# Kernel optimization log

Hardware: AMD Instinct MI355X
Metric: run time of the kernel (lower is better)

The kernel has to match this reference:

```python
import jax, jax.numpy as jnp
import numpy as np

N_NODES = 50000


def setup_inputs() -> dict:
    key = jax.random.key(0)
    ks = jax.random.split(key, 6)
    nfeat, nhid, hops, nedges = 256, 64, 4, 800000
    x = jax.random.normal(ks[0], (N_NODES, nfeat), dtype=jnp.float32)
    W = jax.random.normal(ks[1], (hops, nfeat, nhid), dtype=jnp.float32) / np.sqrt(nfeat)
    b = jax.random.normal(ks[2], (hops, nhid), dtype=jnp.float32) * 0.01
    adj_rows = jax.random.randint(ks[3], (hops, nedges), 0, N_NODES, dtype=jnp.int32)
    adj_cols = jax.random.randint(ks[4], (hops, nedges), 0, N_NODES, dtype=jnp.int32)
    # normalize-ish positive edge weights, as in a GCN-normalized adjacency
    adj_vals = jax.random.uniform(ks[5], (hops, nedges), dtype=jnp.float32) / 16.0
    return {"x": x, "W": W, "b": b, "adj_rows": adj_rows,
            "adj_cols": adj_cols, "adj_vals": adj_vals}


def reference(x, W, b, adj_rows, adj_cols, adj_vals):
    # SIGN forward (eval mode: dropout = identity).
    # For each hop i: h = x @ W[i] + b[i]; out_i = spmm(adj_i, h)
    # spmm in COO form: out[r] = sum_{e: rows[e]==r} vals[e] * h[cols[e]]
    n = x.shape[0]
    hops = W.shape[0]
    outs = []
    for i in range(hops):  # small fixed hop count (layers+1)
        h = x @ W[i] + b[i]                      # [N, nhid] dense GEMM
        msgs = adj_vals[i][:, None] * h[adj_cols[i]]  # [E, nhid] gather
        outs.append(jax.ops.segment_sum(msgs, adj_rows[i], num_segments=n))
    return jax.nn.elu(jnp.concatenate(outs, axis=1))  # [N, hops*nhid]
```

## Files before the change

kernel.cpp:

```cpp
#include <hip/hip_runtime.h>
#include <hip/hip_bf16.h>
#include <math.h>

#define N_NODES 50000
#define NFEAT 256
#define NHID 64
#define HOPS 4
#define NEDGES 800000
#define NBINS (HOPS * N_NODES)

#define BROWS 64
#define NBUCK 782
#define NBK_ALL (HOPS * NBUCK)
#define CHUNK 4096
#define NCHUNK ((NEDGES + CHUNK - 1) / CHUNK)
#define FS_CAP 2048
#define MCAP 512

#define GM 64
#define LDP 40
#define NGBLK ((N_NODES + GM - 1) / GM)

#define PREP_BHIST (NCHUNK * HOPS)
#define PREP_CASTW_END (PREP_BHIST + 256)
#define PREP_CASTX_BLKS ((N_NODES * NFEAT / 8) / 256)
#define PREP_TOTAL (PREP_CASTW_END + PREP_CASTX_BLKS)

typedef short bf16x8 __attribute__((ext_vector_type(8)));
typedef float f32x4 __attribute__((ext_vector_type(4)));

static __device__ __forceinline__ unsigned short f2bf(float f) {
    __hip_bfloat16 h = __float2bfloat16(f);
    return *reinterpret_cast<unsigned short*>(&h);
}

__global__ __launch_bounds__(256) void prep_kernel(const float* __restrict__ x,
                                                   unsigned short* __restrict__ Xbf,
                                                   const float* __restrict__ W,
                                                   unsigned short* __restrict__ Wt,
                                                   const int* __restrict__ rows,
                                                   int* __restrict__ bucket_cnt) {
    __shared__ int h[NBUCK];
    const int bid = blockIdx.x;
    const int t = threadIdx.x;

    if (bid < PREP_BHIST) {
        for (int i = t; i < NBUCK; i += 256) h[i] = 0;
        __syncthreads();
        const int hop = bid / NCHUNK;
        const int e0 = (bid % NCHUNK) * CHUNK;
        const int n = min(CHUNK, NEDGES - e0);
        const size_t base = (size_t)hop * NEDGES + e0;
        for (int i = t; i < n; i += 256) {
            atomicAdd(&h[rows[base + i] >> 6], 1);
        }
        __syncthreads();
        for (int i = t; i < NBUCK; i += 256) {
            if (h[i]) atomicAdd(&bucket_cnt[hop * NBUCK + i], h[i]);
        }
    } else if (bid < PREP_CASTW_END) {
        const int idx = (bid - PREP_BHIST) * 256 + t;
        const int hop = idx >> 14;
        const int k = (idx >> 6) & 255;
        const int c = idx & 63;
        Wt[(size_t)(k >> 5) * (256 * 32) + (hop * 64 + c) * 32 + (k & 31)] = f2bf(W[idx]);
    } else {
        const size_t base = ((size_t)(bid - PREP_CASTW_END) * 256 + t) * 8;
        const float4 a = *(const float4*)&x[base];
        const float4 c = *(const float4*)&x[base + 4];
        unsigned short o[8] = {f2bf(a.x), f2bf(a.y), f2bf(a.z), f2bf(a.w),
                               f2bf(c.x), f2bf(c.y), f2bf(c.z), f2bf(c.w)};
        *(bf16x8*)&Xbf[base] = *(const bf16x8*)o;
    }
}

#define SCAN_V ((NBK_ALL + 255) / 256)
__global__ __launch_bounds__(256) void gemm_scan_kernel(const unsigned short* __restrict__ Xbf,
                                                        const unsigned short* __restrict__ Wt,
                                                        const float* __restrict__ b,
                                                        __hip_bfloat16* __restrict__ H,
                                                        const int* __restrict__ cnt,
                                                        int* __restrict__ start,
                                                        int* __restrict__ cursor,
                                                        int* __restrict__ offsets) {
    __shared__ char smem[GM * LDP * 2 + 256 * LDP * 2];
    const int t = threadIdx.x;

    if (blockIdx.x == 0) {
        int* s = (int*)smem;
        int v[SCAN_V];
        int tsum = 0;
#pragma unroll
        for (int i = 0; i < SCAN_V; ++i) {
            const int idx = t * SCAN_V + i;
            v[i] = (idx < NBK_ALL) ? cnt[idx] : 0;
            tsum += v[i];
        }
        s[t] = tsum;
        __syncthreads();
        for (int off = 1; off < 256; off <<= 1) {
            const int a = (t >= off) ? s[t - off] : 0;
            __syncthreads();
            s[t] += a;
            __syncthreads();
        }
        int run = s[t] - tsum;
#pragma unroll
        for (int i = 0; i < SCAN_V; ++i) {
            const int idx = t * SCAN_V + i;
            if (idx < NBK_ALL) {
                start[idx] = run;
                cursor[idx] = run;
                run += v[i];
            }
        }
        if (t == 255) {
            start[NBK_ALL] = run;
            offsets[NBINS] = run;
        }
        return;
    }

    unsigned short* A_lds = (unsigned short*)smem;
    unsigned short* B_lds = (unsigned short*)(smem + GM * LDP * 2);

    const int lane = t & 63;
    const int w = t >> 6;
    const int quad = lane >> 4;
    const int m16 = lane & 15;
    const int row0 = (blockIdx.x - 1) * GM;

    f32x4 acc[4][4];
#pragma unroll
    for (int mt = 0; mt < 4; ++mt)
#pragma unroll
        for (int nt = 0; nt < 4; ++nt) acc[mt][nt] = (f32x4){0.f, 0.f, 0.f, 0.f};

    for (int ks = 0; ks < 8; ++ks) {
        const int k0 = ks * 32;
        {
            const int r = t >> 2;
            const int kq = (t & 3) * 8;
            bf16x8 v = {0, 0, 0, 0, 0, 0, 0, 0};
            if (row0 + r < N_NODES)
                v = *(const bf16x8*)&Xbf[(size_t)(row0 + r) * NFEAT + k0 + kq];
            *(bf16x8*)&A_lds[r * LDP + kq] = v;
        }
#pragma unroll
        for (int it = 0; it < 4; ++it) {
            const int i = t + it * 256;
            const bf16x8 v = *(const bf16x8*)&Wt[(size_t)ks * (256 * 32) + (size_t)i * 8];
            *(bf16x8*)&B_lds[(i >> 2) * LDP + (i & 3) * 8] = v;
        }
        __syncthreads();

        bf16x8 af[4], bf[4];
#pragma unroll
        for (int mt = 0; mt < 4; ++mt)
            af[mt] = *(const bf16x8*)&A_lds[(mt * 16 + m16) * LDP + quad * 8];
#pragma unroll
        for (int nt = 0; nt < 4; ++nt)
            bf[nt] = *(const bf16x8*)&B_lds[(w * 64 + nt * 16 + m16) * LDP + quad * 8];
#pragma unroll
        for (int mt = 0; mt < 4; ++mt)
#pragma unroll
            for (int nt = 0; nt < 4; ++nt)
                acc[mt][nt] = __builtin_amdgcn_mfma_f32_16x16x32_bf16(
                    af[mt], bf[nt], acc[mt][nt], 0, 0, 0);
        __syncthreads();
    }

#pragma unroll
    for (int nt = 0; nt < 4; ++nt) {
        const int col = w * 64 + nt * 16 + m16;
        const float bias = b[col];
#pragma unroll
        for (int mt = 0; mt < 4; ++mt) {
#pragma unroll
            for (int r = 0; r < 4; ++r) {
                const int row = row0 + mt * 16 + quad * 4 + r;
                if (row < N_NODES)
                    H[(size_t)row * 256 + col] = __float2bfloat16(acc[mt][nt][r] + bias);
            }
        }
    }
}

__global__ __launch_bounds__(256) void gemm_mfma_kernel(const float* __restrict__ x,
                                                        const float* __restrict__ W,
                                                        const float* __restrict__ b,
                                                        __hip_bfloat16* __restrict__ H) {
    __shared__ unsigned short A_lds[GM * LDP];
    __shared__ unsigned short B_lds[256 * LDP];

    const int t = threadIdx.x;
    const int lane = t & 63;
    const int w = t >> 6;
    const int quad = lane >> 4;
    const int m16 = lane & 15;
    const int row0 = blockIdx.x * GM;

    f32x4 acc[4][4];
#pragma unroll
    for (int mt = 0; mt < 4; ++mt)
#pragma unroll
        for (int nt = 0; nt < 4; ++nt) acc[mt][nt] = (f32x4){0.f, 0.f, 0.f, 0.f};

    for (int ks = 0; ks < 8; ++ks) {
        const int k0 = ks * 32;
#pragma unroll
        for (int it = 0; it < 2; ++it) {
            const int i = t + it * 256;
            const int r = i >> 3;
            const int kq = (i & 7) * 4;
            float4 v = make_float4(0.f, 0.f, 0.f, 0.f);
            if (row0 + r < N_NODES)
                v = *(const float4*)&x[(size_t)(row0 + r) * NFEAT + k0 + kq];
            unsigned short* d = &A_lds[r * LDP + kq];
            d[0] = f2bf(v.x); d[1] = f2bf(v.y); d[2] = f2bf(v.z); d[3] = f2bf(v.w);
        }
#pragma unroll
        for (int it = 0; it < 8; ++it) {
            const int i = t + it * 256;
            const int n4 = i & 63;
            const int kk = i >> 6;
            const int hop = n4 >> 4;
            const int j = (n4 & 15) * 4;
            const float4 v = *(const float4*)&W[(size_t)hop * (NFEAT * NHID)
                                                + (size_t)(k0 + kk) * NHID + j];
            B_lds[(n4 * 4 + 0) * LDP + kk] = f2bf(v.x);
            B_lds[(n4 * 4 + 1) * LDP + kk] = f2bf(v.y);
            B_lds[(n4 * 4 + 2) * LDP + kk] = f2bf(v.z);
            B_lds[(n4 * 4 + 3) * LDP + kk] = f2bf(v.w);
        }
        __syncthreads();

        bf16x8 af[4], bf[4];
#pragma unroll
        for (int mt = 0; mt < 4; ++mt)
            af[mt] = *(const bf16x8*)&A_lds[(mt * 16 + m16) * LDP + quad * 8];
#pragma unroll
        for (int nt = 0; nt < 4; ++nt)
            bf[nt] = *(const bf16x8*)&B_lds[(w * 64 + nt * 16 + m16) * LDP + quad * 8];
#pragma unroll
        for (int mt = 0; mt < 4; ++mt)
#pragma unroll
            for (int nt = 0; nt < 4; ++nt)
                acc[mt][nt] = __builtin_amdgcn_mfma_f32_16x16x32_bf16(
                    af[mt], bf[nt], acc[mt][nt], 0, 0, 0);
        __syncthreads();
    }

#pragma unroll
    for (int nt = 0; nt < 4; ++nt) {
        const int col = w * 64 + nt * 16 + m16;
        const float bias = b[col];
#pragma unroll
        for (int mt = 0; mt < 4; ++mt) {
#pragma unroll
            for (int r = 0; r < 4; ++r) {
                const int row = row0 + mt * 16 + quad * 4 + r;
                if (row < N_NODES)
                    H[(size_t)row * 256 + col] = __float2bfloat16(acc[mt][nt][r] + bias);
            }
        }
    }
}

__global__ __launch_bounds__(256) void partition_kernel(const int* __restrict__ rows,
                                                        const int* __restrict__ cols,
                                                        const float* __restrict__ vals,
                                                        int* __restrict__ cursor,
                                                        int2* __restrict__ partbuf) {
    __shared__ int2 pay[CHUNK];
    __shared__ int h[NBUCK], excl[NBUCK], gbase[NBUCK], lcur[NBUCK];
    __shared__ int s[256];
    const int t = threadIdx.x;
    const int hop = blockIdx.y;
    const int e0 = blockIdx.x * CHUNK;
    const int n = min(CHUNK, NEDGES - e0);
    const size_t base = (size_t)hop * NEDGES + e0;

    for (int i = t; i < NBUCK; i += 256) h[i] = 0;
    __syncthreads();

    int myrow[CHUNK / 256];
#pragma unroll
    for (int j = 0; j < CHUNK / 256; ++j) {
        const int i = t + j * 256;
        if (i < n) {
            const int r = rows[base + i];
            myrow[j] = r;
            atomicAdd(&h[r >> 6], 1);
        }
    }
    __syncthreads();

    int pv[4];
    int tsum = 0;
#pragma unroll
    for (int i = 0; i < 4; ++i) {
        const int idx = t * 4 + i;
        pv[i] = (idx < NBUCK) ? h[idx] : 0;
        tsum += pv[i];
    }
    s[t] = tsum;
    __syncthreads();
    for (int off = 1; off < 256; off <<= 1) {
        const int a = (t >= off) ? s[t - off] : 0;
        __syncthreads();
        s[t] += a;
        __syncthreads();
    }
    int run = s[t] - tsum;
#pragma unroll
    for (int i = 0; i < 4; ++i) {
        const int idx = t * 4 + i;
        if (idx < NBUCK) {
            excl[idx] = run;
            lcur[idx] = run;
            gbase[idx] = pv[i] ? atomicAdd(&cursor[hop * NBUCK + idx], pv[i]) : 0;
            run += pv[i];
        }
    }
    __syncthreads();

#pragma unroll
    for (int j = 0; j < CHUNK / 256; ++j) {
        const int i = t + j * 256;
        if (i < n) {
            const int r = myrow[j];
            const int c = cols[base + i];
            const float v = vals[base + i];
            const int pos = atomicAdd(&lcur[r >> 6], 1);
            pay[pos] = make_int2((r << 16) | c, __float_as_int(v));
        }
    }
    __syncthreads();

    for (int i = t; i < n; i += 256) {
        const int2 p = pay[i];
        const int bk = ((unsigned)p.x) >> 22;
        partbuf[gbase[bk] + (i - excl[bk])] = p;
    }
}

__global__ __launch_bounds__(256) void fsort_kernel(const int* __restrict__ start,
                                                    int2* __restrict__ partbuf,
                                                    int* __restrict__ offsets) {
    __shared__ int2 pay[FS_CAP];
    __shared__ int h[BROWS], excl[BROWS], cur[BROWS];
    __shared__ int s[256];
    const int t = threadIdx.x;
    const int hop = blockIdx.y;
    const int bucket = blockIdx.x;
    const int g = hop * NBUCK + bucket;
    const int s0 = start[g];
    const int n = min(start[g + 1] - s0, FS_CAP);

    if (t < BROWS) h[t] = 0;
    __syncthreads();

    for (int i = t; i < n; i += 256) {
        const int2 p = partbuf[s0 + i];
        pay[i] = p;
        atomicAdd(&h[((unsigned)p.x >> 16) & (BROWS - 1)], 1);
    }
    __syncthreads();

    const int hv = (t < BROWS) ? h[t] : 0;
    s[t] = hv;
    __syncthreads();
    for (int off = 1; off < 256; off <<= 1) {
        const int a = (t >= off) ? s[t - off] : 0;
        __syncthreads();
        s[t] += a;
        __syncthreads();
    }
    if (t < BROWS) {
        const int ex = s[t] - hv;
        excl[t] = ex;
        cur[t] = 0;
        const int row = bucket * BROWS + t;
        if (row < N_NODES) offsets[hop * N_NODES + row] = s0 + ex;
    }
    __syncthreads();

    for (int i = t; i < n; i += 256) {
        const int2 p = pay[i];
        const int rl = ((unsigned)p.x >> 16) & (BROWS - 1);
        const int pos = s0 + excl[rl] + atomicAdd(&cur[rl], 1);
        partbuf[pos] = make_int2(p.x & 0xFFFF, p.y);
    }
}

__global__ __launch_bounds__(256) void csr_gather_kernel(const __hip_bfloat16* __restrict__ H,
                                                         const int* __restrict__ offsets,
                                                         const int2* __restrict__ epk,
                                                         float* __restrict__ out) {
    __shared__ int2 meta[4][MCAP + 16];
    const int t = threadIdx.x;
    const int f = t & 63;
    const int w = t >> 6;
    const int hop = blockIdx.y;
    const int row0w = blockIdx.x * 64 + w * 16;
    if (row0w >= N_NODES) return;
    const int bin0 = hop * N_NODES + row0w;

    int off_l = 0;
    if (f <= 16) off_l = offsets[bin0 + f];
    const int s0w = __builtin_amdgcn_readlane(off_l, 0);
    const int s1w = __builtin_amdgcn_readlane(off_l, 16);
    const int cnt = s1w - s0w;

    if (cnt <= MCAP) {
        const int gi = f >> 5;
        const int fp = f & 31;
        const char* Hb = (const char*)H + hop * 128 + fp * 4;
        float* outp = out + (size_t)row0w * 256 + hop * 64 + fp * 2;

        int2* M = meta[w];
        for (int i = f; i < cnt; i += 64) M[i] = epk[s0w + i];
        if (f < 16) M[cnt + f] = make_int2(0, 0);

        for (int r = 0; r < 16; ++r) {
            const int s  = __builtin_amdgcn_readlane(off_l, r) - s0w;
            const int e2 = __builtin_amdgcn_readlane(off_l, r + 1) - s0w;
            float aLo = 0.f, aHi = 0.f;
            for (int g = s; g < e2; g += 16) {
                int2 mm[8];
#pragma unroll
                for (int j = 0; j < 8; ++j) mm[j] = M[g + gi * 8 + j];
                unsigned hv[8];
#pragma unroll
                for (int j = 0; j < 8; ++j) {
                    hv[j] = *(const unsigned*)(Hb + ((size_t)(unsigned)mm[j].x << 9));
                }
#pragma unroll
                for (int j = 0; j < 8; ++j) {
                    const float vj = (g + gi * 8 + j < e2) ? __int_as_float(mm[j].y) : 0.f;
                    aLo = fmaf(vj, __uint_as_float(hv[j] << 16), aLo);
                    aHi = fmaf(vj, __uint_as_float(hv[j] & 0xffff0000u), aHi);
                }
            }
            aLo += __shfl_xor(aLo, 32, 64);
            aHi += __shfl_xor(aHi, 32, 64);
            aLo = aLo > 0.f ? aLo : __expf(aLo) - 1.f;
            aHi = aHi > 0.f ? aHi : __expf(aHi) - 1.f;
            if (f < 32)
                *(float2*)(outp + (size_t)r * 256) = make_float2(aLo, aHi);
        }
    } else {
        const unsigned short* Hf = (const unsigned short*)H + hop * 64 + f;
        float* outp = out + (size_t)row0w * 256 + hop * 64 + f;
        for (int r = 0; r < 16; ++r) {
            const int s  = __builtin_amdgcn_readlane(off_l, r);
            const int e2 = __builtin_amdgcn_readlane(off_l, r + 1);
            float acc = 0.f;
            int e = s;
            for (; e + 8 <= e2; e += 8) {
                const int2 m = epk[e + (f & 7)];
                float h8[8];
#pragma unroll
                for (int j = 0; j < 8; ++j) {
                    const int col = __builtin_amdgcn_readlane(m.x, j);
                    h8[j] = __uint_as_float((unsigned)Hf[(size_t)col << 8] << 16);
                }
#pragma unroll
                for (int j = 0; j < 8; ++j) {
                    const float val =
                        __uint_as_float((unsigned)__builtin_amdgcn_readlane(m.y, j));
                    acc = fmaf(val, h8[j], acc);
                }
            }
            if (e < e2) {
                const int2 m = epk[e + (f & 7)];
                const int rem = e2 - e;
                for (int j = 0; j < rem; ++j) {
                    const int col = __builtin_amdgcn_readlane(m.x, j);
                    const float val =
                        __uint_as_float((unsigned)__builtin_amdgcn_readlane(m.y, j));
                    acc = fmaf(val, __uint_as_float((unsigned)Hf[(size_t)col << 8] << 16),
                               acc);
                }
            }
            acc = acc > 0.f ? acc : __expf(acc) - 1.f;
            outp[(size_t)r * 256] = acc;
        }
    }
}

#define EPW 8
__global__ __launch_bounds__(256) void scatter_kernel(const __hip_bfloat16* __restrict__ H,
                                                      const int* __restrict__ rows,
                                                      const int* __restrict__ cols,
                                                      const float* __restrict__ vals,
                                                      float* __restrict__ out) {
    const int lane = threadIdx.x & 63;
    const int wid = __builtin_amdgcn_readfirstlane(threadIdx.x >> 6);
    const int hop = blockIdx.y;
    const int e0 = (blockIdx.x * 4 + wid) * EPW;
    const int base = hop * NEDGES;
    const int hoff = hop * 64 + lane;
#pragma unroll
    for (int i = 0; i < EPW; ++i) {
        const int e = e0 + i;
        const int r = rows[base + e];
        const int c = cols[base + e];
        const float v = vals[base + e];
        unsafeAtomicAdd(&out[(size_t)r * 256 + hoff],
                        v * __bfloat162float(H[(size_t)c * 256 + hoff]));
    }
}

__global__ __launch_bounds__(256) void elu_kernel(float* __restrict__ out, int n4) {
    const int i = blockIdx.x * 256 + threadIdx.x;
    if (i < n4) {
        float4 v = ((float4*)out)[i];
        v.x = v.x > 0.f ? v.x : expf(v.x) - 1.f;
        v.y = v.y > 0.f ? v.y : expf(v.y) - 1.f;
        v.z = v.z > 0.f ? v.z : expf(v.z) - 1.f;
        v.w = v.w > 0.f ? v.w : expf(v.w) - 1.f;
        ((float4*)out)[i] = v;
    }
}

extern "C" void kernel_launch(void* const* d_in, const int* in_sizes, int n_in,
                              void* d_out, int out_size, void* d_ws, size_t ws_size,
                              hipStream_t stream) {
    const float* x        = (const float*)d_in[0];
    const float* W        = (const float*)d_in[1];
    const float* b        = (const float*)d_in[2];
    const int*   adj_rows = (const int*)d_in[3];
    const int*   adj_cols = (const int*)d_in[4];
    const float* adj_vals = (const float*)d_in[5];
    float* out = (float*)d_out;

    char* w = (char*)d_ws;
    size_t off = 0;
    __hip_bfloat16* H = (__hip_bfloat16*)(w + off);
    off += (size_t)N_NODES * 256 * 2;
    int2*  partbuf    = (int2*)(w + off);  off += (size_t)HOPS * NEDGES * 8;
    int*   offsets    = (int*)(w + off);   off += (((size_t)(NBINS + 1)) * 4 + 255) & ~255ull;
    int*   bucket_cnt = (int*)(w + off);   off += ((size_t)NBK_ALL * 4 + 255) & ~255ull;
    int*   bstart     = (int*)(w + off);   off += (((size_t)NBK_ALL + 1) * 4 + 255) & ~255ull;
    int*   bcursor    = (int*)(w + off);   off += ((size_t)NBK_ALL * 4 + 255) & ~255ull;
    const bool use_sorted = (ws_size >= off);

    unsigned short* Xbf = (unsigned short*)partbuf;
    unsigned short* Wt  = (unsigned short*)offsets;

    if (use_sorted) {
        hipMemsetAsync(bucket_cnt, 0, (size_t)NBK_ALL * 4, stream);
        prep_kernel<<<PREP_TOTAL, 256, 0, stream>>>(x, Xbf, W, Wt, adj_rows, bucket_cnt);
        gemm_scan_kernel<<<NGBLK + 1, 256, 0, stream>>>(Xbf, Wt, b, H,
                                                        bucket_cnt, bstart, bcursor, offsets);
        partition_kernel<<<dim3(NCHUNK, HOPS), 256, 0, stream>>>(adj_rows, adj_cols,
                                                                 adj_vals, bcursor, partbuf);
        fsort_kernel<<<dim3(NBUCK, HOPS), 256, 0, stream>>>(bstart, partbuf, offsets);
        csr_gather_kernel<<<dim3((N_NODES + 63) / 64, HOPS), 256, 0, stream>>>(
            H, offsets, partbuf, out);
    } else {
        gemm_mfma_kernel<<<NGBLK, 256, 0, stream>>>(x, W, b, H);
        hipMemsetAsync(d_out, 0, (size_t)out_size * sizeof(float), stream);
        scatter_kernel<<<dim3(NEDGES / (4 * EPW), HOPS), 256, 0, stream>>>(
            H, adj_rows, adj_cols, adj_vals, out);
        elu_kernel<<<(out_size / 4 + 255) / 256, 256, 0, stream>>>(out, out_size / 4);
    }
}
```

Baseline: 317.6 us.

## Replace two-level bucket sort with direct per-row counting-sort CSR build

```diff
diff --git a/kernel.cpp b/kernel.cpp
--- a/kernel.cpp
+++ b/kernel.cpp
@@ -9,20 +9,17 @@
 #define NEDGES 800000
 #define NBINS (HOPS * N_NODES)
 
-#define BROWS 64
-#define NBUCK 782
-#define NBK_ALL (HOPS * NBUCK)
 #define CHUNK 4096
 #define NCHUNK ((NEDGES + CHUNK - 1) / CHUNK)
-#define FS_CAP 2048
 #define MCAP 512
+#define NTILE ((NBINS + 1023) / 1024)
 
 #define GM 64
 #define LDP 40
 #define NGBLK ((N_NODES + GM - 1) / GM)
 
-#define PREP_BHIST (NCHUNK * HOPS)
-#define PREP_CASTW_END (PREP_BHIST + 256)
+#define PREP_RHIST (NCHUNK * HOPS)
+#define PREP_CASTW_END (PREP_RHIST + 256)
 #define PREP_CASTX_BLKS ((N_NODES * NFEAT / 8) / 256)
 #define PREP_TOTAL (PREP_CASTW_END + PREP_CASTX_BLKS)
 
@@ -39,27 +36,21 @@
                                                    const float* __restrict__ W,
                                                    unsigned short* __restrict__ Wt,
                                                    const int* __restrict__ rows,
-                                                   int* __restrict__ bucket_cnt) {
-    __shared__ int h[NBUCK];
+                                                   int* __restrict__ cnt) {
     const int bid = blockIdx.x;
     const int t = threadIdx.x;
 
-    if (bid < PREP_BHIST) {
-        for (int i = t; i < NBUCK; i += 256) h[i] = 0;
-        __syncthreads();
+    if (bid < PREP_RHIST) {
         const int hop = bid / NCHUNK;
         const int e0 = (bid % NCHUNK) * CHUNK;
         const int n = min(CHUNK, NEDGES - e0);
         const size_t base = (size_t)hop * NEDGES + e0;
+        const int binb = hop * N_NODES;
         for (int i = t; i < n; i += 256) {
-            atomicAdd(&h[rows[base + i] >> 6], 1);
-        }
-        __syncthreads();
-        for (int i = t; i < NBUCK; i += 256) {
-            if (h[i]) atomicAdd(&bucket_cnt[hop * NBUCK + i], h[i]);
+            atomicAdd(&cnt[binb + rows[base + i]], 1);
         }
     } else if (bid < PREP_CASTW_END) {
-        const int idx = (bid - PREP_BHIST) * 256 + t;
+        const int idx = (bid - PREP_RHIST) * 256 + t;
         const int hop = idx >> 14;
         const int k = (idx >> 6) & 255;
         const int c = idx & 63;
@@ -74,29 +65,29 @@
     }
 }
 
-#define SCAN_V ((NBK_ALL + 255) / 256)
 __global__ __launch_bounds__(256) void gemm_scan_kernel(const unsigned short* __restrict__ Xbf,
                                                         const unsigned short* __restrict__ Wt,
                                                         const float* __restrict__ b,
                                                         __hip_bfloat16* __restrict__ H,
                                                         const int* __restrict__ cnt,
-                                                        int* __restrict__ start,
-                                                        int* __restrict__ cursor,
-                                                        int* __restrict__ offsets) {
+                                                        int* __restrict__ offsets,
+                                                        int* __restrict__ tsum) {
     __shared__ char smem[GM * LDP * 2 + 256 * LDP * 2];
     const int t = threadIdx.x;
 
-    if (blockIdx.x == 0) {
+    if (blockIdx.x < NTILE) {
         int* s = (int*)smem;
-        int v[SCAN_V];
-        int tsum = 0;
-#pragma unroll
-        for (int i = 0; i < SCAN_V; ++i) {
-            const int idx = t * SCAN_V + i;
-            v[i] = (idx < NBK_ALL) ? cnt[idx] : 0;
-            tsum += v[i];
-        }
-        s[t] = tsum;
+        const int j = blockIdx.x;
+        const int i0 = j * 1024 + t * 4;
+        int c[4];
+        int tl = 0;
+#pragma unroll
+        for (int i = 0; i < 4; ++i) {
+            const int idx = i0 + i;
+            c[i] = (idx < NBINS) ? cnt[idx] : 0;
+            tl += c[i];
+        }
+        s[t] = tl;
         __syncthreads();
         for (int off = 1; off < 256; off <<= 1) {
             const int a = (t >= off) ? s[t - off] : 0;
@@ -104,20 +95,14 @@
             s[t] += a;
             __syncthreads();
         }
-        int run = s[t] - tsum;
-#pragma unroll
-        for (int i = 0; i < SCAN_V; ++i) {
-            const int idx = t * SCAN_V + i;
-            if (idx < NBK_ALL) {
-                start[idx] = run;
-                cursor[idx] = run;
-                run += v[i];
-            }
-        }
-        if (t == 255) {
-            start[NBK_ALL] = run;
-            offsets[NBINS] = run;
-        }
+        int run = s[t] - tl;
+#pragma unroll
+        for (int i = 0; i < 4; ++i) {
+            const int idx = i0 + i;
+            if (idx <= NBINS) offsets[idx] = run;
+            run += c[i];
+        }
+        if (t == 255) tsum[j] = run;
         return;
     }
 
@@ -128,7 +113,7 @@
     const int w = t >> 6;
     const int quad = lane >> 4;
     const int m16 = lane & 15;
-    const int row0 = (blockIdx.x - 1) * GM;
+    const int row0 = (blockIdx.x - NTILE) * GM;
 
     f32x4 acc[4][4];
 #pragma unroll
@@ -182,6 +167,56 @@
                 if (row < N_NODES)
                     H[(size_t)row * 256 + col] = __float2bfloat16(acc[mt][nt][r] + bias);
             }
+        }
+    }
+}
+
+__global__ __launch_bounds__(256) void fixup_kernel(const int* __restrict__ tsum,
+                                                    int* __restrict__ offsets,
+                                                    int* __restrict__ cursor) {
+    __shared__ int s[256];
+    const int t = threadIdx.x;
+    const int j = blockIdx.x;
+    const int own = (t < NTILE) ? tsum[t] : 0;
+    s[t] = own;
+    __syncthreads();
+    for (int off = 1; off < 256; off <<= 1) {
+        const int a = (t >= off) ? s[t - off] : 0;
+        __syncthreads();
+        s[t] += a;
+        __syncthreads();
+    }
+    const int base = (j > 0) ? s[j - 1] : 0;
+    const int i0 = j * 1024 + t * 4;
+#pragma unroll
+    for (int i = 0; i < 4; ++i) {
+        const int idx = i0 + i;
+        if (idx <= NBINS) {
+            const int v = offsets[idx] + base;
+            offsets[idx] = v;
+            if (idx < NBINS) cursor[idx] = v;
+        }
+    }
+}
+
+__global__ __launch_bounds__(256) void place_kernel(const int* __restrict__ rows,
+                                                    const int* __restrict__ cols,
+                                                    const float* __restrict__ vals,
+                                                    int* __restrict__ cursor,
+                                                    int2* __restrict__ partbuf) {
+    const int t = threadIdx.x;
+    const int hop = blockIdx.y;
+    const int e0 = blockIdx.x * CHUNK;
+    const int n = min(CHUNK, NEDGES - e0);
+    const size_t base = (size_t)hop * NEDGES + e0;
+    const int binb = hop * N_NODES;
+#pragma unroll
+    for (int k = 0; k < CHUNK / 256; ++k) {
+        const int i = t + k * 256;
+        if (i < n) {
+            const int r = rows[base + i];
+            const int pos = atomicAdd(&cursor[binb + r], 1);
+            partbuf[pos] = make_int2(cols[base + i], __float_as_int(vals[base + i]));
         }
     }
 }
@@ -264,133 +299,6 @@
                     H[(size_t)row * 256 + col] = __float2bfloat16(acc[mt][nt][r] + bias);
             }
         }
-    }
-}
-
-__global__ __launch_bounds__(256) void partition_kernel(const int* __restrict__ rows,
-                                                        const int* __restrict__ cols,
-                                                        const float* __restrict__ vals,
-                                                        int* __restrict__ cursor,
-                                                        int2* __restrict__ partbuf) {
-    __shared__ int2 pay[CHUNK];
-    __shared__ int h[NBUCK], excl[NBUCK], gbase[NBUCK], lcur[NBUCK];
-    __shared__ int s[256];
-    const int t = threadIdx.x;
-    const int hop = blockIdx.y;
-    const int e0 = blockIdx.x * CHUNK;
-    const int n = min(CHUNK, NEDGES - e0);
-    const size_t base = (size_t)hop * NEDGES + e0;
-
-    for (int i = t; i < NBUCK; i += 256) h[i] = 0;
-    __syncthreads();
-
-    int myrow[CHUNK / 256];
-#pragma unroll
-    for (int j = 0; j < CHUNK / 256; ++j) {
-        const int i = t + j * 256;
-        if (i < n) {
-            const int r = rows[base + i];
-            myrow[j] = r;
-            atomicAdd(&h[r >> 6], 1);
-        }
-    }
-    __syncthreads();
-
-    int pv[4];
-    int tsum = 0;
-#pragma unroll
-    for (int i = 0; i < 4; ++i) {
-        const int idx = t * 4 + i;
-        pv[i] = (idx < NBUCK) ? h[idx] : 0;
-        tsum += pv[i];
-    }
-    s[t] = tsum;
-    __syncthreads();
-    for (int off = 1; off < 256; off <<= 1) {
-        const int a = (t >= off) ? s[t - off] : 0;
-        __syncthreads();
-        s[t] += a;
-        __syncthreads();
-    }
-    int run = s[t] - tsum;
-#pragma unroll
-    for (int i = 0; i < 4; ++i) {
-        const int idx = t * 4 + i;
-        if (idx < NBUCK) {
-            excl[idx] = run;
-            lcur[idx] = run;
-            gbase[idx] = pv[i] ? atomicAdd(&cursor[hop * NBUCK + idx], pv[i]) : 0;
-            run += pv[i];
-        }
-    }
-    __syncthreads();
-
-#pragma unroll
-    for (int j = 0; j < CHUNK / 256; ++j) {
-        const int i = t + j * 256;
-        if (i < n) {
-            const int r = myrow[j];
-            const int c = cols[base + i];
-            const float v = vals[base + i];
-            const int pos = atomicAdd(&lcur[r >> 6], 1);
-            pay[pos] = make_int2((r << 16) | c, __float_as_int(v));
-        }
-    }
-    __syncthreads();
-
-    for (int i = t; i < n; i += 256) {
-        const int2 p = pay[i];
-        const int bk = ((unsigned)p.x) >> 22;
-        partbuf[gbase[bk] + (i - excl[bk])] = p;
-    }
-}
-
-__global__ __launch_bounds__(256) void fsort_kernel(const int* __restrict__ start,
-                                                    int2* __restrict__ partbuf,
-                                                    int* __restrict__ offsets) {
-    __shared__ int2 pay[FS_CAP];
-    __shared__ int h[BROWS], excl[BROWS], cur[BROWS];
-    __shared__ int s[256];
-    const int t = threadIdx.x;
-    const int hop = blockIdx.y;
-    const int bucket = blockIdx.x;
-    const int g = hop * NBUCK + bucket;
-    const int s0 = start[g];
-    const int n = min(start[g + 1] - s0, FS_CAP);
-
-    if (t < BROWS) h[t] = 0;
-    __syncthreads();
-
-    for (int i = t; i < n; i += 256) {
-        const int2 p = partbuf[s0 + i];
-        pay[i] = p;
-        atomicAdd(&h[((unsigned)p.x >> 16) & (BROWS - 1)], 1);
-    }
-    __syncthreads();
-
-    const int hv = (t < BROWS) ? h[t] : 0;
-    s[t] = hv;
-    __syncthreads();
-    for (int off = 1; off < 256; off <<= 1) {
-        const int a = (t >= off) ? s[t - off] : 0;
-        __syncthreads();
-        s[t] += a;
-        __syncthreads();
-    }
-    if (t < BROWS) {
-        const int ex = s[t] - hv;
-        excl[t] = ex;
-        cur[t] = 0;
-        const int row = bucket * BROWS + t;
-        if (row < N_NODES) offsets[hop * N_NODES + row] = s0 + ex;
-    }
-    __syncthreads();
-
-    for (int i = t; i < n; i += 256) {
-        const int2 p = pay[i];
-        const int rl = ((unsigned)p.x >> 16) & (BROWS - 1);
-        const int pos = s0 + excl[rl] + atomicAdd(&cur[rl], 1);
-        partbuf[pos] = make_int2(p.x & 0xFFFF, p.y);
     }
 }
 
@@ -540,24 +448,25 @@
     size_t off = 0;
     __hip_bfloat16* H = (__hip_bfloat16*)(w + off);
     off += (size_t)N_NODES * 256 * 2;
-    int2*  partbuf    = (int2*)(w + off);  off += (size_t)HOPS * NEDGES * 8;
-    int*   offsets    = (int*)(w + off);   off += (((size_t)(NBINS + 1)) * 4 + 255) & ~255ull;
-    int*   bucket_cnt = (int*)(w + off);   off += ((size_t)NBK_ALL * 4 + 255) & ~255ull;
-    int*   bstart     = (int*)(w + off);   off += (((size_t)NBK_ALL + 1) * 4 + 255) & ~255ull;
-    int*   bcursor    = (int*)(w + off);   off += ((size_t)NBK_ALL * 4 + 255) & ~255ull;
+    int2*  partbuf = (int2*)(w + off);  off += (size_t)HOPS * NEDGES * 8;
+    int*   offsets = (int*)(w + off);   off += (((size_t)(NBINS + 1)) * 4 + 255) & ~255ull;
+    int*   cnt     = (int*)(w + off);   off += ((size_t)NBINS * 4 + 255) & ~255ull;
+    int*   cursor  = (int*)(w + off);   off += ((size_t)NBINS * 4 + 255) & ~255ull;
+    int*   tsum    = (int*)(w + off);   off += ((size_t)NTILE * 4 + 255) & ~255ull;
+    unsigned short* Wt = (unsigned short*)(w + off);
+    off += (size_t)HOPS * NFEAT * NHID * 2;
     const bool use_sorted = (ws_size >= off);
 
     unsigned short* Xbf = (unsigned short*)partbuf;
-    unsigned short* Wt  = (unsigned short*)offsets;
 
     if (use_sorted) {
-        hipMemsetAsync(bucket_cnt, 0, (size_t)NBK_ALL * 4, stream);
-        prep_kernel<<<PREP_TOTAL, 256, 0, stream>>>(x, Xbf, W, Wt, adj_rows, bucket_cnt);
-        gemm_scan_kernel<<<NGBLK + 1, 256, 0, stream>>>(Xbf, Wt, b, H,
-                                                        bucket_cnt, bstart, bcursor, offsets);
-        partition_kernel<<<dim3(NCHUNK, HOPS), 256, 0, stream>>>(adj_rows, adj_cols,
-                                                                 adj_vals, bcursor, partbuf);
-        fsort_kernel<<<dim3(NBUCK, HOPS), 256, 0, stream>>>(bstart, partbuf, offsets);
+        hipMemsetAsync(cnt, 0, (size_t)NBINS * 4, stream);
+        prep_kernel<<<PREP_TOTAL, 256, 0, stream>>>(x, Xbf, W, Wt, adj_rows, cnt);
+        gemm_scan_kernel<<<NTILE + NGBLK, 256, 0, stream>>>(Xbf, Wt, b, H,
+                                                            cnt, offsets, tsum);
+        fixup_kernel<<<NTILE, 256, 0, stream>>>(tsum, offsets, cursor);
+        place_kernel<<<dim3(NCHUNK, HOPS), 256, 0, stream>>>(adj_rows, adj_cols,
+                                                             adj_vals, cursor, partbuf);
         csr_gather_kernel<<<dim3((N_NODES + 63) / 64, HOPS), 256, 0, stream>>>(
             H, offsets, partbuf, out);
     } else {
```

Result: slower. 531.5 us (+67.3%).
